# Optimization experiments

Measured on AMD Instinct MI355X. Metric: run time of the kernel, lower is better.

The kernel has to match this reference:

```python
import jax, jax.numpy as jnp
import numpy as np

B, H, W, C = 4, 256, 256, 256
WS = 8          # window size (both dims)
HEADS = 1
SEQ = WS * WS   # 64 tokens per window
NW = B * (H // WS) * (W // WS)  # 4096 windows
INNER = C * HEADS


def setup_inputs() -> dict:
    key = jax.random.key(0)
    k1, k2, k3, k4 = jax.random.split(key, 4)
    x = jax.random.normal(k1, (B, H, W, C), dtype=jnp.float32)
    attn = jax.random.uniform(k2, (NW, HEADS, SEQ, SEQ), dtype=jnp.float32)
    # to_v: Linear(dim, inner_dim, bias=False); stored as [in, out] for x @ Wv
    Wv = jax.random.normal(k3, (C, INNER), dtype=jnp.float32) * (C ** -0.5)
    # to_out: Linear(inner_dim, dim)
    Wo = jax.random.normal(k4, (INNER, C), dtype=jnp.float32) * (INNER ** -0.5)
    bo = jnp.zeros((C,), dtype=jnp.float32)
    return {"x": x, "attn": attn, "Wv": Wv, "Wo": Wo, "bo": bo}


def reference(x, attn, Wv, Wo, bo):
    b, h, w, c = x.shape
    nh, nw = h // WS, w // WS
    # window partition: b (h b0) (w b1) c -> (b h w) (b0 b1) c
    xw = x.reshape(b, nh, WS, nw, WS, c).transpose(0, 1, 3, 2, 4, 5)
    xw = xw.reshape(b * nh * nw, SEQ, c)
    # value projection, split heads: n s (h d) -> n h s d
    v = (xw @ Wv).reshape(-1, SEQ, HEADS, c).transpose(0, 2, 1, 3)
    # precomputed-attention weighted sum
    out = jnp.einsum('nhij,nhjd->nhid', attn, v)
    # merge heads: n h s d -> n s (h d)
    out = out.transpose(0, 2, 1, 3).reshape(-1, SEQ, HEADS * c)
    out = out @ Wo + bo
    # window un-partition: (b h w) (b0 b1) c -> b (h b0) (w b1) c
    out = out.reshape(b, nh, nw, WS, WS, c).transpose(0, 1, 3, 2, 4, 5)
    return out.reshape(b, h, w, c)
```

## Files before the change

### kernel.cpp

```cpp
#include <hip/hip_runtime.h>
#include <hip/hip_bf16.h>


typedef __bf16 bf16x8 __attribute__((ext_vector_type(8)));
typedef __bf16 bf16x4 __attribute__((ext_vector_type(4)));
typedef float  f32x16 __attribute__((ext_vector_type(16)));
typedef float  f32x4  __attribute__((ext_vector_type(4)));
typedef unsigned int uint;
typedef uint   uint4v __attribute__((ext_vector_type(4)));

#define MFMA32(a, b, c) __builtin_amdgcn_mfma_f32_32x32x16_bf16(a, b, c, 0, 0, 0)

__global__ void wfuse_kernel(const float* __restrict__ Wv,
                             const float* __restrict__ Wo,
                             __bf16* __restrict__ WT) {
  const int n = blockIdx.x;
  const int k = threadIdx.x;
  const float* wvrow = Wv + k * 256;
  float acc = 0.f;
#pragma unroll 4
  for (int j = 0; j < 256; j += 4) {
    f32x4 wv = *(const f32x4*)(wvrow + j);
    acc += wv.x * Wo[(j + 0) * 256 + n];
    acc += wv.y * Wo[(j + 1) * 256 + n];
    acc += wv.z * Wo[(j + 2) * 256 + n];
    acc += wv.w * Wo[(j + 3) * 256 + n];
  }
  WT[n * 256 + k] = (__bf16)acc;
}

static __device__ __forceinline__ uint pkbf(float lo, float hi) {
  return (uint)__builtin_bit_cast(unsigned short, (__bf16)lo) |
         ((uint)__builtin_bit_cast(unsigned short, (__bf16)hi) << 16);
}

static __device__ __forceinline__ void build_bfrags(const f32x16 acc, int lh,
                                                    bf16x8* bf) {
  uint wd0 = pkbf(acc[0],  acc[1]);
  uint wd1 = pkbf(acc[2],  acc[3]);
  uint wd2 = pkbf(acc[4],  acc[5]);
  uint wd3 = pkbf(acc[6],  acc[7]);
  uint wd4 = pkbf(acc[8],  acc[9]);
  uint wd5 = pkbf(acc[10], acc[11]);
  uint wd6 = pkbf(acc[12], acc[13]);
  uint wd7 = pkbf(acc[14], acc[15]);
  {
    uint o0 = (uint)__shfl_xor((int)wd2, 32);
    uint o1 = (uint)__shfl_xor((int)wd3, 32);
    uint o2 = (uint)__shfl_xor((int)wd0, 32);
    uint o3 = (uint)__shfl_xor((int)wd1, 32);
    uint4v uv = { lh ? o0 : wd0, lh ? o1 : wd1,
                  lh ? wd2 : o2, lh ? wd3 : o3 };
    bf[0] = __builtin_bit_cast(bf16x8, uv);
  }
  {
    uint o0 = (uint)__shfl_xor((int)wd6, 32);
    uint o1 = (uint)__shfl_xor((int)wd7, 32);
    uint o2 = (uint)__shfl_xor((int)wd4, 32);
    uint o3 = (uint)__shfl_xor((int)wd5, 32);
    uint4v uv = { lh ? o0 : wd4, lh ? o1 : wd5,
                  lh ? wd6 : o2, lh ? wd7 : o3 };
    bf[1] = __builtin_bit_cast(bf16x8, uv);
  }
}

__global__ __launch_bounds__(512, 6)
void na_msa_kernel(const float* __restrict__ x,
                   const float* __restrict__ attn,
                   const __bf16* __restrict__ WT,
                   const float* __restrict__ bo,
                   float* __restrict__ out) {
  __shared__ char lds[40960];
  char* lds_xw = lds;
  char* lds_at = lds + 32768;

  const int t    = threadIdx.x;
  const int lane = t & 63;
  const int wvi  = t >> 6;
  const int ln31 = lane & 31;
  const int lh   = lane >> 5;

  const int n  = blockIdx.x;
  const int wi = n & 31;
  const int hi = (n >> 5) & 31;
  const int b  = n >> 10;
  const long base = (((long)(b * 256 + hi * 8)) * 256 + wi * 8) * 256;
  const float* xp = x + base;
  const float* ap = attn + (long)n * 4096;

#pragma unroll
  for (int i = 0; i < 8; ++i) {
    int gi = i * 512 + t;
    int rowblk = gi >> 9;
    int f = gi & 511;
    f32x4 v = *(const f32x4*)(xp + rowblk * 65536 + f * 4);
    int tok = rowblk * 8 + (f >> 6);
    int ch0 = (f & 63) * 4;
    bf16x4 hv = { (__bf16)v.x, (__bf16)v.y, (__bf16)v.z, (__bf16)v.w };
    *(bf16x4*)(lds_xw + tok * 512 + ((ch0 * 2) ^ ((tok & 31) << 4))) = hv;
  }
#pragma unroll
  for (int i = 0; i < 2; ++i) {
    int fi = i * 512 + t;
    f32x4 v = *(const f32x4*)(ap + fi * 4);
    int row = fi >> 4;
    int k0 = (fi & 15) * 4;
    bf16x4 hv = { (__bf16)v.x, (__bf16)v.y, (__bf16)v.z, (__bf16)v.w };
    *(bf16x4*)(lds_at + row * 128 + ((k0 * 2) ^ ((row & 7) << 4))) = hv;
  }
  __syncthreads();

  f32x16 acc0 = {}, acc1 = {};
  const __bf16* wtp = WT + (wvi * 32 + ln31) * 256 + 8 * lh;
#pragma unroll 2
  for (int ks = 0; ks < 16; ++ks) {
    int kk = ks * 16 + 8 * lh;
    int byt0 = ln31 * 512 + ((kk * 2) ^ (ln31 << 4));
    bf16x8 a0 = *(const bf16x8*)(lds_xw + byt0);
    bf16x8 a1 = *(const bf16x8*)(lds_xw + byt0 + 16384);
    bf16x8 b0 = *(const bf16x8*)(wtp + ks * 16);
    acc0 = MFMA32(a0, b0, acc0);
    acc1 = MFMA32(a1, b0, acc1);
  }

  bf16x8 bfr[4];
  build_bfrags(acc0, lh, &bfr[0]);
  build_bfrags(acc1, lh, &bfr[2]);

  f32x16 o0 = {}, o1 = {};
#pragma unroll
  for (int ks = 0; ks < 4; ++ks) {
    int kk = ks * 16 + 8 * lh;
    int ab0 = ln31 * 128 + ((kk * 2) ^ ((ln31 & 7) << 4));
    bf16x8 a0 = *(const bf16x8*)(lds_at + ab0);
    bf16x8 a1 = *(const bf16x8*)(lds_at + ab0 + 4096);
    o0 = MFMA32(a0, bfr[ks], o0);
    o1 = MFMA32(a1, bfr[ks], o1);
  }

  float* op = out + base;
  const int ch = wvi * 32 + ln31;
  const float bv = bo[ch];
#pragma unroll
  for (int r = 0; r < 16; ++r) {
    int tok = (r & 3) + 8 * (r >> 2) + 4 * lh;
    op[(tok >> 3) * 65536 + (tok & 7) * 256 + ch] = o0[r] + bv;
  }
#pragma unroll
  for (int r = 0; r < 16; ++r) {
    int tok = 32 + (r & 3) + 8 * (r >> 2) + 4 * lh;
    op[(tok >> 3) * 65536 + (tok & 7) * 256 + ch] = o1[r] + bv;
  }
}

extern "C" void kernel_launch(void* const* d_in, const int* in_sizes, int n_in,
                              void* d_out, int out_size, void* d_ws, size_t ws_size,
                              hipStream_t stream) {
  const float* x    = (const float*)d_in[0];
  const float* attn = (const float*)d_in[1];
  const float* Wv   = (const float*)d_in[2];
  const float* Wo   = (const float*)d_in[3];
  const float* bo   = (const float*)d_in[4];
  float* out = (float*)d_out;
  __bf16* WT = (__bf16*)d_ws;

  wfuse_kernel<<<256, 256, 0, stream>>>(Wv, Wo, WT);
  na_msa_kernel<<<4096, 512, 0, stream>>>(x, attn, WT, bo, out);
}
```

Measured before the change: 173.4 us.

## Process four windows per block with double-buffered LDS prefetch of next window

Each block now handles four consecutive windows instead of one and double-buffers the LDS tiles. Global loads for the next window are issued into registers before the current window's MFMAs and written to the alternate buffer afterwards, so memory latency overlaps with compute. The grid shrinks to 1024 blocks and LDS per block doubles, with occupancy pinned to 4 waves per EU, which lowers concurrent blocks and may hurt latency hiding for this memory-bound kernel.

```diff
diff --git a/kernel.cpp b/kernel.cpp
--- a/kernel.cpp
+++ b/kernel.cpp
@@ -64,15 +64,21 @@
   }
 }
 
-__global__ __launch_bounds__(512, 6)
+static __device__ __forceinline__ long wbase(int w) {
+  int wi = w & 31;
+  int hi = (w >> 5) & 31;
+  int b  = w >> 10;
+  return (((long)(b * 256 + hi * 8)) * 256 + wi * 8) * 256;
+}
+
+__global__ __launch_bounds__(512)
+__attribute__((amdgpu_waves_per_eu(4, 4)))
 void na_msa_kernel(const float* __restrict__ x,
                    const float* __restrict__ attn,
                    const __bf16* __restrict__ WT,
                    const float* __restrict__ bo,
                    float* __restrict__ out) {
-  __shared__ char lds[40960];
-  char* lds_xw = lds;
-  char* lds_at = lds + 32768;
+  __shared__ char lds[81920];
 
   const int t    = threadIdx.x;
   const int lane = t & 63;
@@ -80,76 +86,132 @@
   const int ln31 = lane & 31;
   const int lh   = lane >> 5;
 
-  const int n  = blockIdx.x;
-  const int wi = n & 31;
-  const int hi = (n >> 5) & 31;
-  const int b  = n >> 10;
-  const long base = (((long)(b * 256 + hi * 8)) * 256 + wi * 8) * 256;
-  const float* xp = x + base;
-  const float* ap = attn + (long)n * 4096;
-
+  const int tq   = t >> 6;
+  const int xch0 = (t & 63) * 4;
+  const int arow0 = t >> 4;
+  const int ak0  = (t & 15) * 4;
+
+  const __bf16* wtp = WT + (wvi * 32 + ln31) * 256 + 8 * lh;
+  const float bv = bo[wvi * 32 + ln31];
+
+  const int w0 = blockIdx.x * 4;
+
+#define XBYT(J)  ((((J) * 8 + tq) * 512) + ((xch0 * 2) ^ (((((J) * 8 + tq)) & 31) << 4)))
+#define ABYT(I)  (((I) * 32 + arow0) * 128 + ((ak0 * 2) ^ ((((I) * 32 + arow0) & 7) << 4)))
+#define CVT4(V)  bf16x4{ (__bf16)(V).x, (__bf16)(V).y, (__bf16)(V).z, (__bf16)(V).w }
+
+  {
+    const float* xp = x + wbase(w0);
+    const float* ap = attn + (long)w0 * 4096;
+    f32x4 v0 = *(const f32x4*)(xp + 0 * 65536 + t * 4);
+    f32x4 v1 = *(const f32x4*)(xp + 1 * 65536 + t * 4);
+    f32x4 v2 = *(const f32x4*)(xp + 2 * 65536 + t * 4);
+    f32x4 v3 = *(const f32x4*)(xp + 3 * 65536 + t * 4);
+    f32x4 v4 = *(const f32x4*)(xp + 4 * 65536 + t * 4);
+    f32x4 v5 = *(const f32x4*)(xp + 5 * 65536 + t * 4);
+    f32x4 v6 = *(const f32x4*)(xp + 6 * 65536 + t * 4);
+    f32x4 v7 = *(const f32x4*)(xp + 7 * 65536 + t * 4);
+    f32x4 a0 = *(const f32x4*)(ap + t * 4);
+    f32x4 a1 = *(const f32x4*)(ap + (512 + t) * 4);
+    *(bf16x4*)(lds + XBYT(0)) = CVT4(v0);
+    *(bf16x4*)(lds + XBYT(1)) = CVT4(v1);
+    *(bf16x4*)(lds + XBYT(2)) = CVT4(v2);
+    *(bf16x4*)(lds + XBYT(3)) = CVT4(v3);
+    *(bf16x4*)(lds + XBYT(4)) = CVT4(v4);
+    *(bf16x4*)(lds + XBYT(5)) = CVT4(v5);
+    *(bf16x4*)(lds + XBYT(6)) = CVT4(v6);
+    *(bf16x4*)(lds + XBYT(7)) = CVT4(v7);
+    *(bf16x4*)(lds + 32768 + ABYT(0)) = CVT4(a0);
+    *(bf16x4*)(lds + 32768 + ABYT(1)) = CVT4(a1);
+  }
+  asm volatile("s_waitcnt lgkmcnt(0)" ::: "memory");
+  __builtin_amdgcn_s_barrier();
+  __builtin_amdgcn_sched_barrier(0);
+
+#pragma unroll 1
+  for (int i = 0; i < 4; ++i) {
+    const int w = w0 + i;
+    char* lds_xw = lds + (i & 1) * 40960;
+    char* lds_at = lds_xw + 32768;
+
+    f32x4 px0, px1, px2, px3, px4, px5, px6, px7, pa0, pa1;
+    if (i < 3) {
+      const float* xp = x + wbase(w + 1);
+      const float* ap = attn + (long)(w + 1) * 4096;
+      px0 = *(const f32x4*)(xp + 0 * 65536 + t * 4);
+      px1 = *(const f32x4*)(xp + 1 * 65536 + t * 4);
+      px2 = *(const f32x4*)(xp + 2 * 65536 + t * 4);
+      px3 = *(const f32x4*)(xp + 3 * 65536 + t * 4);
+      px4 = *(const f32x4*)(xp + 4 * 65536 + t * 4);
+      px5 = *(const f32x4*)(xp + 5 * 65536 + t * 4);
+      px6 = *(const f32x4*)(xp + 6 * 65536 + t * 4);
+      px7 = *(const f32x4*)(xp + 7 * 65536 + t * 4);
+      pa0 = *(const f32x4*)(ap + t * 4);
+      pa1 = *(const f32x4*)(ap + (512 + t) * 4);
+    }
+    __builtin_amdgcn_sched_barrier(0);
+
+    f32x16 acc0 = {}, acc1 = {};
+#pragma unroll 2
+    for (int ks = 0; ks < 16; ++ks) {
+      int kk = ks * 16 + 8 * lh;
+      int byt0 = ln31 * 512 + ((kk * 2) ^ (ln31 << 4));
+      bf16x8 a0 = *(const bf16x8*)(lds_xw + byt0);
+      bf16x8 a1 = *(const bf16x8*)(lds_xw + byt0 + 16384);
+      bf16x8 b0 = *(const bf16x8*)(wtp + ks * 16);
+      acc0 = MFMA32(a0, b0, acc0);
+      acc1 = MFMA32(a1, b0, acc1);
+    }
+    __builtin_amdgcn_sched_barrier(0);
+
+    bf16x8 bfr[4];
+    build_bfrags(acc0, lh, &bfr[0]);
+    build_bfrags(acc1, lh, &bfr[2]);
+
+    if (i < 3) {
+      char* bxw = lds + ((i + 1) & 1) * 40960;
+      char* bat = bxw + 32768;
+      *(bf16x4*)(bxw + XBYT(0)) = CVT4(px0);
+      *(bf16x4*)(bxw + XBYT(1)) = CVT4(px1);
+      *(bf16x4*)(bxw + XBYT(2)) = CVT4(px2);
+      *(bf16x4*)(bxw + XBYT(3)) = CVT4(px3);
+      *(bf16x4*)(bxw + XBYT(4)) = CVT4(px4);
+      *(bf16x4*)(bxw + XBYT(5)) = CVT4(px5);
+      *(bf16x4*)(bxw + XBYT(6)) = CVT4(px6);
+      *(bf16x4*)(bxw + XBYT(7)) = CVT4(px7);
+      *(bf16x4*)(bat + ABYT(0)) = CVT4(pa0);
+      *(bf16x4*)(bat + ABYT(1)) = CVT4(pa1);
+    }
+
+    f32x16 o0 = {}, o1 = {};
 #pragma unroll
-  for (int i = 0; i < 8; ++i) {
-    int gi = i * 512 + t;
-    int rowblk = gi >> 9;
-    int f = gi & 511;
-    f32x4 v = *(const f32x4*)(xp + rowblk * 65536 + f * 4);
-    int tok = rowblk * 8 + (f >> 6);
-    int ch0 = (f & 63) * 4;
-    bf16x4 hv = { (__bf16)v.x, (__bf16)v.y, (__bf16)v.z, (__bf16)v.w };
-    *(bf16x4*)(lds_xw + tok * 512 + ((ch0 * 2) ^ ((tok & 31) << 4))) = hv;
-  }
+    for (int ks = 0; ks < 4; ++ks) {
+      int kk = ks * 16 + 8 * lh;
+      int ab0 = ln31 * 128 + ((kk * 2) ^ ((ln31 & 7) << 4));
+      bf16x8 a0 = *(const bf16x8*)(lds_at + ab0);
+      bf16x8 a1 = *(const bf16x8*)(lds_at + ab0 + 4096);
+      o0 = MFMA32(a0, bfr[ks], o0);
+      o1 = MFMA32(a1, bfr[ks], o1);
+    }
+
+    {
+      float* op = out + wbase(w);
+      const int ch = wvi * 32 + ln31;
 #pragma unroll
-  for (int i = 0; i < 2; ++i) {
-    int fi = i * 512 + t;
-    f32x4 v = *(const f32x4*)(ap + fi * 4);
-    int row = fi >> 4;
-    int k0 = (fi & 15) * 4;
-    bf16x4 hv = { (__bf16)v.x, (__bf16)v.y, (__bf16)v.z, (__bf16)v.w };
-    *(bf16x4*)(lds_at + row * 128 + ((k0 * 2) ^ ((row & 7) << 4))) = hv;
-  }
-  __syncthreads();
-
-  f32x16 acc0 = {}, acc1 = {};
-  const __bf16* wtp = WT + (wvi * 32 + ln31) * 256 + 8 * lh;
-#pragma unroll 2
-  for (int ks = 0; ks < 16; ++ks) {
-    int kk = ks * 16 + 8 * lh;
-    int byt0 = ln31 * 512 + ((kk * 2) ^ (ln31 << 4));
-    bf16x8 a0 = *(const bf16x8*)(lds_xw + byt0);
-    bf16x8 a1 = *(const bf16x8*)(lds_xw + byt0 + 16384);
-    bf16x8 b0 = *(const bf16x8*)(wtp + ks * 16);
-    acc0 = MFMA32(a0, b0, acc0);
-    acc1 = MFMA32(a1, b0, acc1);
-  }
-
-  bf16x8 bfr[4];
-  build_bfrags(acc0, lh, &bfr[0]);
-  build_bfrags(acc1, lh, &bfr[2]);
-
-  f32x16 o0 = {}, o1 = {};
+      for (int r = 0; r < 16; ++r) {
+        int tok = (r & 3) + 8 * (r >> 2) + 4 * lh;
+        op[(tok >> 3) * 65536 + (tok & 7) * 256 + ch] = o0[r] + bv;
+      }
 #pragma unroll
-  for (int ks = 0; ks < 4; ++ks) {
-    int kk = ks * 16 + 8 * lh;
-    int ab0 = ln31 * 128 + ((kk * 2) ^ ((ln31 & 7) << 4));
-    bf16x8 a0 = *(const bf16x8*)(lds_at + ab0);
-    bf16x8 a1 = *(const bf16x8*)(lds_at + ab0 + 4096);
-    o0 = MFMA32(a0, bfr[ks], o0);
-    o1 = MFMA32(a1, bfr[ks], o1);
-  }
-
-  float* op = out + base;
-  const int ch = wvi * 32 + ln31;
-  const float bv = bo[ch];
-#pragma unroll
-  for (int r = 0; r < 16; ++r) {
-    int tok = (r & 3) + 8 * (r >> 2) + 4 * lh;
-    op[(tok >> 3) * 65536 + (tok & 7) * 256 + ch] = o0[r] + bv;
-  }
-#pragma unroll
-  for (int r = 0; r < 16; ++r) {
-    int tok = 32 + (r & 3) + 8 * (r >> 2) + 4 * lh;
-    op[(tok >> 3) * 65536 + (tok & 7) * 256 + ch] = o1[r] + bv;
+      for (int r = 0; r < 16; ++r) {
+        int tok = 32 + (r & 3) + 8 * (r >> 2) + 4 * lh;
+        op[(tok >> 3) * 65536 + (tok & 7) * 256 + ch] = o1[r] + bv;
+      }
+    }
+
+    asm volatile("s_waitcnt lgkmcnt(0)" ::: "memory");
+    __builtin_amdgcn_s_barrier();
+    __builtin_amdgcn_sched_barrier(0);
   }
 }
 
@@ -165,5 +227,5 @@
   __bf16* WT = (__bf16*)d_ws;
 
   wfuse_kernel<<<256, 256, 0, stream>>>(Wv, Wo, WT);
-  na_msa_kernel<<<4096, 512, 0, stream>>>(x, attn, WT, bo, out);
-}
+  na_msa_kernel<<<1024, 512, 0, stream>>>(x, attn, WT, bo, out);
+}
```

New measurement: 180.9 us. +4.3%, slower.

## Make window kernel persistent with double-buffered async global-to-LDS prefetch

Applied to the files above, without the earlier changes.

Each block now processes 16 windows in a loop. It prefetches the next window's x tile into a double-buffered LDS region with global_load_lds DMA (kept fp32, converted to bf16 when read) and its attention tile via registers, while computing the current window. The goal is to overlap memory traffic with MFMA compute and to amortise per-block setup. In exchange it uses 144KB of LDS, which limits occupancy to one block per CU, and the grid shrinks to 256 blocks.

```diff
diff --git a/kernel.cpp b/kernel.cpp
--- a/kernel.cpp
+++ b/kernel.cpp
@@ -64,15 +64,36 @@
   }
 }
 
-__global__ __launch_bounds__(512, 6)
+static __device__ __forceinline__ long wbase(int w) {
+  int wi = w & 31;
+  int hi = (w >> 5) & 31;
+  int b  = w >> 10;
+  return (((long)(b * 256 + hi * 8)) * 256 + wi * 8) * 256;
+}
+
+static __device__ __forceinline__ void dma16(const float* gp, char* lp) {
+  __builtin_amdgcn_global_load_lds(
+      (const __attribute__((address_space(1))) uint*)gp,
+      (__attribute__((address_space(3))) uint*)lp, 16, 0, 0);
+}
+
+static __device__ __forceinline__ bf16x8 ldax(const char* xs, int tok, int g) {
+  const int sw = tok & 31;
+  f32x4 u = *(const f32x4*)(xs + tok * 1024 + ((g ^ sw) << 4));
+  f32x4 v = *(const f32x4*)(xs + tok * 1024 + (((g + 1) ^ sw) << 4));
+  bf16x8 r;
+  r[0] = (__bf16)u.x; r[1] = (__bf16)u.y; r[2] = (__bf16)u.z; r[3] = (__bf16)u.w;
+  r[4] = (__bf16)v.x; r[5] = (__bf16)v.y; r[6] = (__bf16)v.z; r[7] = (__bf16)v.w;
+  return r;
+}
+
+__global__ __launch_bounds__(512)
 void na_msa_kernel(const float* __restrict__ x,
                    const float* __restrict__ attn,
                    const __bf16* __restrict__ WT,
                    const float* __restrict__ bo,
                    float* __restrict__ out) {
-  __shared__ char lds[40960];
-  char* lds_xw = lds;
-  char* lds_at = lds + 32768;
+  __shared__ char lds[147456];
 
   const int t    = threadIdx.x;
   const int lane = t & 63;
@@ -80,77 +101,111 @@
   const int ln31 = lane & 31;
   const int lh   = lane >> 5;
 
-  const int n  = blockIdx.x;
-  const int wi = n & 31;
-  const int hi = (n >> 5) & 31;
-  const int b  = n >> 10;
-  const long base = (((long)(b * 256 + hi * 8)) * 256 + wi * 8) * 256;
-  const float* xp = x + base;
-  const float* ap = attn + (long)n * 4096;
-
+  const __bf16* wtp = WT + (wvi * 32 + ln31) * 256 + 8 * lh;
+  const float bv = bo[wvi * 32 + ln31];
+
+  const int arow0 = t >> 4;
+  const int ak0   = (t & 15) * 4;
+
+  const int w0 = blockIdx.x * 16;
+
+#define STAGE_X(W, BUFOFF) do {                                            \
+    const float* xp_ = x + wbase(W);                                       \
+    _Pragma("unroll")                                                      \
+    for (int j = 0; j < 8; ++j) {                                          \
+      int tok_ = j * 8 + wvi;                                              \
+      int ch0_ = (lane ^ (tok_ & 31)) * 4;                                 \
+      const float* gp_ = xp_ + (tok_ >> 3) * 65536 + (tok_ & 7) * 256 + ch0_; \
+      int off_ = __builtin_amdgcn_readfirstlane((BUFOFF) + j * 8192 + wvi * 1024); \
+      dma16(gp_, lds + off_);                                              \
+    } } while (0)
+
+  STAGE_X(w0, 0);
+  {
+    const float* ap = attn + (long)w0 * 4096;
+    f32x4 a0 = *(const f32x4*)(ap + t * 4);
+    f32x4 a1 = *(const f32x4*)(ap + (512 + t) * 4);
+    char* bat = lds + 131072;
+    *(bf16x4*)(bat + arow0 * 128 + ((ak0 * 2) ^ ((arow0 & 7) << 4))) =
+        bf16x4{ (__bf16)a0.x, (__bf16)a0.y, (__bf16)a0.z, (__bf16)a0.w };
+    int row1 = 32 + arow0;
+    *(bf16x4*)(bat + row1 * 128 + ((ak0 * 2) ^ ((row1 & 7) << 4))) =
+        bf16x4{ (__bf16)a1.x, (__bf16)a1.y, (__bf16)a1.z, (__bf16)a1.w };
+  }
+  asm volatile("s_waitcnt vmcnt(0) lgkmcnt(0)" ::: "memory");
+  __builtin_amdgcn_s_barrier();
+  __builtin_amdgcn_sched_barrier(0);
+
+#pragma unroll 1
+  for (int i = 0; i < 16; ++i) {
+    const int w = w0 + i;
+    const char* xs = lds + (i & 1) * 65536;
+    const char* as = lds + 131072 + (i & 1) * 8192;
+
+    f32x4 ra0, ra1;
+    if (i < 15) {
+      const float* ap = attn + (long)(w + 1) * 4096;
+      ra0 = *(const f32x4*)(ap + t * 4);
+      ra1 = *(const f32x4*)(ap + (512 + t) * 4);
+      STAGE_X(w + 1, ((i + 1) & 1) * 65536);
+    }
+    __builtin_amdgcn_sched_barrier(0);
+
+    f32x16 acc0 = {}, acc1 = {};
+#pragma unroll 4
+    for (int ks = 0; ks < 16; ++ks) {
+      int g = 4 * ks + 2 * lh;
+      bf16x8 a0 = ldax(xs, ln31, g);
+      bf16x8 a1 = ldax(xs, 32 + ln31, g);
+      bf16x8 b0 = *(const bf16x8*)(wtp + ks * 16);
+      acc0 = MFMA32(a0, b0, acc0);
+      acc1 = MFMA32(a1, b0, acc1);
+    }
+
+    bf16x8 bfr[4];
+    build_bfrags(acc0, lh, &bfr[0]);
+    build_bfrags(acc1, lh, &bfr[2]);
+
+    f32x16 o0 = {}, o1 = {};
 #pragma unroll
-  for (int i = 0; i < 8; ++i) {
-    int gi = i * 512 + t;
-    int rowblk = gi >> 9;
-    int f = gi & 511;
-    f32x4 v = *(const f32x4*)(xp + rowblk * 65536 + f * 4);
-    int tok = rowblk * 8 + (f >> 6);
-    int ch0 = (f & 63) * 4;
-    bf16x4 hv = { (__bf16)v.x, (__bf16)v.y, (__bf16)v.z, (__bf16)v.w };
-    *(bf16x4*)(lds_xw + tok * 512 + ((ch0 * 2) ^ ((tok & 31) << 4))) = hv;
-  }
+    for (int ks = 0; ks < 4; ++ks) {
+      int kk = ks * 16 + 8 * lh;
+      int ab0 = ln31 * 128 + ((kk * 2) ^ ((ln31 & 7) << 4));
+      bf16x8 a0 = *(const bf16x8*)(as + ab0);
+      bf16x8 a1 = *(const bf16x8*)(as + ab0 + 4096);
+      o0 = MFMA32(a0, bfr[ks], o0);
+      o1 = MFMA32(a1, bfr[ks], o1);
+    }
+
+    {
+      float* op = out + wbase(w);
+      const int ch = wvi * 32 + ln31;
 #pragma unroll
-  for (int i = 0; i < 2; ++i) {
-    int fi = i * 512 + t;
-    f32x4 v = *(const f32x4*)(ap + fi * 4);
-    int row = fi >> 4;
-    int k0 = (fi & 15) * 4;
-    bf16x4 hv = { (__bf16)v.x, (__bf16)v.y, (__bf16)v.z, (__bf16)v.w };
-    *(bf16x4*)(lds_at + row * 128 + ((k0 * 2) ^ ((row & 7) << 4))) = hv;
-  }
-  __syncthreads();
-
-  f32x16 acc0 = {}, acc1 = {};
-  const __bf16* wtp = WT + (wvi * 32 + ln31) * 256 + 8 * lh;
-#pragma unroll 2
-  for (int ks = 0; ks < 16; ++ks) {
-    int kk = ks * 16 + 8 * lh;
-    int byt0 = ln31 * 512 + ((kk * 2) ^ (ln31 << 4));
-    bf16x8 a0 = *(const bf16x8*)(lds_xw + byt0);
-    bf16x8 a1 = *(const bf16x8*)(lds_xw + byt0 + 16384);
-    bf16x8 b0 = *(const bf16x8*)(wtp + ks * 16);
-    acc0 = MFMA32(a0, b0, acc0);
-    acc1 = MFMA32(a1, b0, acc1);
-  }
-
-  bf16x8 bfr[4];
-  build_bfrags(acc0, lh, &bfr[0]);
-  build_bfrags(acc1, lh, &bfr[2]);
-
-  f32x16 o0 = {}, o1 = {};
+      for (int r = 0; r < 16; ++r) {
+        int tok = (r & 3) + 8 * (r >> 2) + 4 * lh;
+        op[(tok >> 3) * 65536 + (tok & 7) * 256 + ch] = o0[r] + bv;
+      }
 #pragma unroll
-  for (int ks = 0; ks < 4; ++ks) {
-    int kk = ks * 16 + 8 * lh;
-    int ab0 = ln31 * 128 + ((kk * 2) ^ ((ln31 & 7) << 4));
-    bf16x8 a0 = *(const bf16x8*)(lds_at + ab0);
-    bf16x8 a1 = *(const bf16x8*)(lds_at + ab0 + 4096);
-    o0 = MFMA32(a0, bfr[ks], o0);
-    o1 = MFMA32(a1, bfr[ks], o1);
-  }
-
-  float* op = out + base;
-  const int ch = wvi * 32 + ln31;
-  const float bv = bo[ch];
-#pragma unroll
-  for (int r = 0; r < 16; ++r) {
-    int tok = (r & 3) + 8 * (r >> 2) + 4 * lh;
-    op[(tok >> 3) * 65536 + (tok & 7) * 256 + ch] = o0[r] + bv;
-  }
-#pragma unroll
-  for (int r = 0; r < 16; ++r) {
-    int tok = 32 + (r & 3) + 8 * (r >> 2) + 4 * lh;
-    op[(tok >> 3) * 65536 + (tok & 7) * 256 + ch] = o1[r] + bv;
-  }
+      for (int r = 0; r < 16; ++r) {
+        int tok = 32 + (r & 3) + 8 * (r >> 2) + 4 * lh;
+        op[(tok >> 3) * 65536 + (tok & 7) * 256 + ch] = o1[r] + bv;
+      }
+    }
+
+    if (i < 15) {
+      char* bat = lds + 131072 + ((i + 1) & 1) * 8192;
+      *(bf16x4*)(bat + arow0 * 128 + ((ak0 * 2) ^ ((arow0 & 7) << 4))) =
+          bf16x4{ (__bf16)ra0.x, (__bf16)ra0.y, (__bf16)ra0.z, (__bf16)ra0.w };
+      int row1 = 32 + arow0;
+      *(bf16x4*)(bat + row1 * 128 + ((ak0 * 2) ^ ((row1 & 7) << 4))) =
+          bf16x4{ (__bf16)ra1.x, (__bf16)ra1.y, (__bf16)ra1.z, (__bf16)ra1.w };
+    }
+
+    asm volatile("s_waitcnt vmcnt(0) lgkmcnt(0)" ::: "memory");
+    __builtin_amdgcn_s_barrier();
+    __builtin_amdgcn_sched_barrier(0);
+  }
+#undef STAGE_X
 }
 
 extern "C" void kernel_launch(void* const* d_in, const int* in_sizes, int n_in,
@@ -165,5 +220,5 @@
   __bf16* WT = (__bf16*)d_ws;
 
   wfuse_kernel<<<256, 256, 0, stream>>>(Wv, Wo, WT);
-  na_msa_kernel<<<4096, 512, 0, stream>>>(x, attn, WT, bo, out);
-}
+  na_msa_kernel<<<256, 512, 0, stream>>>(x, attn, WT, bo, out);
+}
```

Measured after the change: 173.2 us. No clear change (-0.1%).

## Drop LDS staging; load x and attn fragments directly from global into MFMA operands

Applied to the files above, without the earlier changes.

Removes the shared-memory staging of the window input and attention tiles. Each wave now reads its own fp32 MFMA A-operand fragments straight from global memory and converts them to bf16 in registers, so the block-wide barrier goes away. The cost is that all 8 waves of a block re-read the same x and attn data, which raises L2/L1 traffic roughly eightfold and relies on cache hits. Launch bounds also drop the occupancy hint of 6.

```diff
diff --git a/kernel.cpp b/kernel.cpp
--- a/kernel.cpp
+++ b/kernel.cpp
@@ -3,7 +3,6 @@
 
 
 typedef __bf16 bf16x8 __attribute__((ext_vector_type(8)));
-typedef __bf16 bf16x4 __attribute__((ext_vector_type(4)));
 typedef float  f32x16 __attribute__((ext_vector_type(16)));
 typedef float  f32x4  __attribute__((ext_vector_type(4)));
 typedef unsigned int uint;
@@ -32,6 +31,13 @@
 static __device__ __forceinline__ uint pkbf(float lo, float hi) {
   return (uint)__builtin_bit_cast(unsigned short, (__bf16)lo) |
          ((uint)__builtin_bit_cast(unsigned short, (__bf16)hi) << 16);
+}
+
+static __device__ __forceinline__ bf16x8 cvt8(f32x4 u, f32x4 v) {
+  bf16x8 r;
+  r[0] = (__bf16)u.x; r[1] = (__bf16)u.y; r[2] = (__bf16)u.z; r[3] = (__bf16)u.w;
+  r[4] = (__bf16)v.x; r[5] = (__bf16)v.y; r[6] = (__bf16)v.z; r[7] = (__bf16)v.w;
+  return r;
 }
 
 static __device__ __forceinline__ void build_bfrags(const f32x16 acc, int lh,
@@ -64,83 +70,68 @@
   }
 }
 
-__global__ __launch_bounds__(512, 6)
+static __device__ __forceinline__ long wbase(int w) {
+  int wi = w & 31;
+  int hi = (w >> 5) & 31;
+  int b  = w >> 10;
+  return (((long)(b * 256 + hi * 8)) * 256 + wi * 8) * 256;
+}
+
+__global__ __launch_bounds__(512)
 void na_msa_kernel(const float* __restrict__ x,
                    const float* __restrict__ attn,
                    const __bf16* __restrict__ WT,
                    const float* __restrict__ bo,
                    float* __restrict__ out) {
-  __shared__ char lds[40960];
-  char* lds_xw = lds;
-  char* lds_at = lds + 32768;
-
   const int t    = threadIdx.x;
   const int lane = t & 63;
   const int wvi  = t >> 6;
   const int ln31 = lane & 31;
   const int lh   = lane >> 5;
 
-  const int n  = blockIdx.x;
-  const int wi = n & 31;
-  const int hi = (n >> 5) & 31;
-  const int b  = n >> 10;
-  const long base = (((long)(b * 256 + hi * 8)) * 256 + wi * 8) * 256;
+  const int w = blockIdx.x;
+  const long base = wbase(w);
   const float* xp = x + base;
-  const float* ap = attn + (long)n * 4096;
+  const float* ap = attn + (long)w * 4096;
 
-#pragma unroll
-  for (int i = 0; i < 8; ++i) {
-    int gi = i * 512 + t;
-    int rowblk = gi >> 9;
-    int f = gi & 511;
-    f32x4 v = *(const f32x4*)(xp + rowblk * 65536 + f * 4);
-    int tok = rowblk * 8 + (f >> 6);
-    int ch0 = (f & 63) * 4;
-    bf16x4 hv = { (__bf16)v.x, (__bf16)v.y, (__bf16)v.z, (__bf16)v.w };
-    *(bf16x4*)(lds_xw + tok * 512 + ((ch0 * 2) ^ ((tok & 31) << 4))) = hv;
-  }
-#pragma unroll
-  for (int i = 0; i < 2; ++i) {
-    int fi = i * 512 + t;
-    f32x4 v = *(const f32x4*)(ap + fi * 4);
-    int row = fi >> 4;
-    int k0 = (fi & 15) * 4;
-    bf16x4 hv = { (__bf16)v.x, (__bf16)v.y, (__bf16)v.z, (__bf16)v.w };
-    *(bf16x4*)(lds_at + row * 128 + ((k0 * 2) ^ ((row & 7) << 4))) = hv;
-  }
-  __syncthreads();
+  const __bf16* wtp = WT + (wvi * 32 + ln31) * 256 + 8 * lh;
+  const float bv = bo[wvi * 32 + ln31];
+
+  const int tokA = ln31, tokB = 32 + ln31;
+  const float* xA = xp + (tokA >> 3) * 65536 + (tokA & 7) * 256 + 8 * lh;
+  const float* xB = xp + (tokB >> 3) * 65536 + (tokB & 7) * 256 + 8 * lh;
 
   f32x16 acc0 = {}, acc1 = {};
-  const __bf16* wtp = WT + (wvi * 32 + ln31) * 256 + 8 * lh;
-#pragma unroll 2
+#pragma unroll
   for (int ks = 0; ks < 16; ++ks) {
-    int kk = ks * 16 + 8 * lh;
-    int byt0 = ln31 * 512 + ((kk * 2) ^ (ln31 << 4));
-    bf16x8 a0 = *(const bf16x8*)(lds_xw + byt0);
-    bf16x8 a1 = *(const bf16x8*)(lds_xw + byt0 + 16384);
+    f32x4 u0 = *(const f32x4*)(xA + ks * 16);
+    f32x4 v0 = *(const f32x4*)(xA + ks * 16 + 4);
+    f32x4 u1 = *(const f32x4*)(xB + ks * 16);
+    f32x4 v1 = *(const f32x4*)(xB + ks * 16 + 4);
     bf16x8 b0 = *(const bf16x8*)(wtp + ks * 16);
-    acc0 = MFMA32(a0, b0, acc0);
-    acc1 = MFMA32(a1, b0, acc1);
+    acc0 = MFMA32(cvt8(u0, v0), b0, acc0);
+    acc1 = MFMA32(cvt8(u1, v1), b0, acc1);
   }
 
   bf16x8 bfr[4];
   build_bfrags(acc0, lh, &bfr[0]);
   build_bfrags(acc1, lh, &bfr[2]);
 
+  const float* aA = ap + tokA * 64 + 8 * lh;
+  const float* aB = ap + tokB * 64 + 8 * lh;
   f32x16 o0 = {}, o1 = {};
 #pragma unroll
   for (int ks = 0; ks < 4; ++ks) {
-    int kk = ks * 16 + 8 * lh;
-    int ab0 = ln31 * 128 + ((kk * 2) ^ ((ln31 & 7) << 4));
-    bf16x8 a0 = *(const bf16x8*)(lds_at + ab0);
-    bf16x8 a1 = *(const bf16x8*)(lds_at + ab0 + 4096);
-    o0 = MFMA32(a0, bfr[ks], o0);
-    o1 = MFMA32(a1, bfr[ks], o1);
+    f32x4 u0 = *(const f32x4*)(aA + ks * 16);
+    f32x4 v0 = *(const f32x4*)(aA + ks * 16 + 4);
+    f32x4 u1 = *(const f32x4*)(aB + ks * 16);
+    f32x4 v1 = *(const f32x4*)(aB + ks * 16 + 4);
+    o0 = MFMA32(cvt8(u0, v0), bfr[ks], o0);
+    o1 = MFMA32(cvt8(u1, v1), bfr[ks], o1);
   }
 
   float* op = out + base;
   const int ch = wvi * 32 + ln31;
-  const float bv = bo[ch];
 #pragma unroll
   for (int r = 0; r < 16; ++r) {
     int tok = (r & 3) + 8 * (r >> 2) + 4 * lh;
```

After: 405.5 us. +133.8%, slower.
